# Kernel optimization log

Measured on AMD Instinct MI355X. Metric: run time of the kernel, lower is better.

## Reference

```python
import jax, jax.numpy as jnp
import numpy as np

EPS = 1e-10
TAU = 1.0


def setup_inputs() -> dict:
    key = jax.random.key(0)
    ks = jax.random.split(key, 5)
    n, d = 1024, 64
    h1, h2, out = 128, 64, 2
    X = jax.random.normal(ks[0], (n, d), dtype=jnp.float32)
    W1 = jax.random.normal(ks[1], (2 * d, h1), dtype=jnp.float32) * (1.0 / np.sqrt(2 * d))
    b1 = jnp.zeros((h1,), dtype=jnp.float32)
    W2 = jax.random.normal(ks[2], (h1, h2), dtype=jnp.float32) * (1.0 / np.sqrt(h1))
    b2 = jnp.zeros((h2,), dtype=jnp.float32)
    W3 = jax.random.normal(ks[3], (h2, out), dtype=jnp.float32) * (1.0 / np.sqrt(h2))
    b3 = jnp.zeros((out,), dtype=jnp.float32)
    u = jax.random.uniform(ks[4], (n, n, out), dtype=jnp.float32)
    return {"X": X, "W1": W1, "b1": b1, "W2": W2, "b2": b2, "W3": W3, "b3": b3, "u": u}


def _mlp(h, W1, b1, W2, b2, W3, b3):
    h = jax.nn.relu(h @ W1 + b1)
    h = jax.nn.relu(h @ W2 + b2)
    return h @ W3 + b3


def reference(X, W1, b1, W2, b2, W3, b3, u):
    n, d = X.shape
    # pairwise features: pair[i, j] = concat(x_i, x_j)  -> (n, n, 2d)
    pair = jnp.concatenate(
        [jnp.broadcast_to(X[:, None, :], (n, n, d)),
         jnp.broadcast_to(X[None, :, :], (n, n, d))], axis=-1)
    logits = _mlp(pair, W1, b1, W2, b2, W3, b3)  # (n, n, 2)
    # undirected: mlp(pair.permute(1,0,2))[i,j] == mlp(pair)[j,i] (row-wise MLP)
    logits = 0.5 * (logits + jnp.swapaxes(logits, 0, 1))
    # gumbel-softmax, hard=True (straight-through)
    g = -jnp.log(-jnp.log(u + EPS) + EPS)
    y_soft = jax.nn.softmax((logits + g) / TAU, axis=-1)
    y_hard = jax.nn.one_hot(jnp.argmax(y_soft, axis=-1), y_soft.shape[-1], dtype=y_soft.dtype)
    y = jax.lax.stop_gradient(y_hard - y_soft) + y_soft
    # narrow(dim=2, start=1, size=1).squeeze() -> adjacency (n, n)
    return y[..., 1]
```

## Files before the change

kernel.cpp:

```cpp
#include <hip/hip_runtime.h>
#include <hip/hip_bf16.h>

#define N 1024
#define D 64
#define H1 128
#define H2 64
#define FLAG_CAP 65536
#define FLAG_THRESH 0.015f
#define H1PAD 136

typedef _Float16 half8 __attribute__((ext_vector_type(8)));
typedef float float4v __attribute__((ext_vector_type(4)));

__global__ __launch_bounds__(128) void precompute_kernel(
    const float* __restrict__ X, const float* __restrict__ W1,
    const float* __restrict__ b1,
    double* __restrict__ A64, double* __restrict__ B64,
    _Float16* __restrict__ A16, _Float16* __restrict__ B16,
    unsigned int* __restrict__ cnt)
{
    if (blockIdx.x == 0 && threadIdx.x == 0) *cnt = 0;
    int i = blockIdx.x;
    int k = threadIdx.x;
    double a = (double)b1[k];
    double b = 0.0;
    for (int c = 0; c < D; ++c) {
        double x = (double)X[i * D + c];
        a += x * (double)W1[c * H1 + k];
        b += x * (double)W1[(D + c) * H1 + k];
    }
    A64[i * H1 + k] = a;
    B64[i * H1 + k] = b;
    A16[i * H1 + k] = (_Float16)(float)a;
    B16[i * H1 + k] = (_Float16)(float)b;
}

__global__ __launch_bounds__(256, 3) void pair_mlp_kernel(
    const _Float16* __restrict__ A16, const _Float16* __restrict__ B16,
    const float* __restrict__ W2, const float* __restrict__ b2,
    const float* __restrict__ W3, float* __restrict__ dmat)
{
    __shared__ _Float16 As16[16 * H1PAD];
    __shared__ _Float16 Bs16[64 * H1PAD];
    __shared__ _Float16 W2t[64 * H1PAD];

    int tid = threadIdx.x;
    int it = blockIdx.x >> 4;
    int jt = blockIdx.x & 15;
    int ti = it << 4;
    int tj = jt << 6;

    {
        int row = tid >> 4;
        int col = (tid & 15) << 3;
        *(half8*)&As16[row * H1PAD + col] =
            *(const half8*)&A16[(size_t)(ti + row) * H1 + col];
    }
    #pragma unroll
    for (int r = 0; r < 4; ++r) {
        int v = tid + r * 256;
        int row = v >> 4;
        int col = (v & 15) << 3;
        *(half8*)&Bs16[row * H1PAD + col] =
            *(const half8*)&B16[(size_t)(tj + row) * H1 + col];
    }
    #pragma unroll
    for (int r = 0; r < 32; ++r) {
        int idx = tid + r * 256;
        int k = idx >> 6;
        int n = idx & 63;
        W2t[n * H1PAD + k] = (_Float16)W2[idx];
    }
    __syncthreads();

    int lane = tid & 63;
    int wave = tid >> 6;
    int quad = lane >> 4;
    int m = lane & 15;

    half8 afrag[4][4];
    #pragma unroll
    for (int ks = 0; ks < 4; ++ks)
        #pragma unroll
        for (int nt = 0; nt < 4; ++nt)
            afrag[ks][nt] = *(const half8*)&W2t[(m + 16 * nt) * H1PAD + quad * 8 + 32 * ks];

    float b2x[4][4], w3x[4][4];
    #pragma unroll
    for (int nt = 0; nt < 4; ++nt)
        #pragma unroll
        for (int reg = 0; reg < 4; ++reg) {
            int o = (quad << 2) + reg + (nt << 4);
            b2x[nt][reg] = b2[o];
            w3x[nt][reg] = W3[o * 2 + 1] - W3[o * 2 + 0];
        }

    const half8 zero8 = {0, 0, 0, 0, 0, 0, 0, 0};

    #pragma unroll 1
    for (int jq = 0; jq < 4; ++jq) {
        int jj0 = jq << 4;
        half8 hb[4];
        #pragma unroll
        for (int ks = 0; ks < 4; ++ks)
            hb[ks] = *(const half8*)&Bs16[(jj0 + m) * H1PAD + quad * 8 + 32 * ks];

        #pragma unroll 1
        for (int i4 = 0; i4 < 4; ++i4) {
            int ii = (wave << 2) + i4;

            float4v acc[4];
            #pragma unroll
            for (int nt = 0; nt < 4; ++nt)
                acc[nt] = (float4v){b2x[nt][0], b2x[nt][1], b2x[nt][2], b2x[nt][3]};

            #pragma unroll
            for (int ks = 0; ks < 4; ++ks) {
                half8 ha = *(const half8*)&As16[ii * H1PAD + quad * 8 + 32 * ks];
                half8 h = __builtin_elementwise_max(ha + hb[ks], zero8);
                #pragma unroll
                for (int nt = 0; nt < 4; ++nt)
                    acc[nt] = __builtin_amdgcn_mfma_f32_16x16x32_f16(afrag[ks][nt], h, acc[nt], 0, 0, 0);
            }

            float s = 0.f;
            #pragma unroll
            for (int nt = 0; nt < 4; ++nt)
                #pragma unroll
                for (int reg = 0; reg < 4; ++reg)
                    s = fmaf(fmaxf(acc[nt][reg], 0.f), w3x[nt][reg], s);
            s += __shfl_xor(s, 16, 64);
            s += __shfl_xor(s, 32, 64);
            if (quad == 0) {
                dmat[(size_t)(ti + ii) * N + (tj + jj0 + m)] = s;
            }
        }
    }
}

__global__ __launch_bounds__(256) void epilogue_kernel(
    const float* __restrict__ dmat, const float* __restrict__ b3,
    const float* __restrict__ u,
    float* __restrict__ out, unsigned int* __restrict__ cnt,
    unsigned int* __restrict__ list)
{
    __shared__ float T1[32][33];
    __shared__ float T2[32][33];
    __shared__ unsigned int lflags[1024];
    __shared__ unsigned int lcnt, lbase;

    int bi = blockIdx.x >> 5;
    int bj = blockIdx.x & 31;
    int i0 = bi * 32, j0 = bj * 32;
    int tid = threadIdx.x;
    int r = tid >> 3;
    int c4 = (tid & 7) << 2;
    if (tid == 0) lcnt = 0;
    *(float4*)&T1[r][c4] = *(const float4*)&dmat[(size_t)(i0 + r) * N + j0 + c4];
    *(float4*)&T2[r][c4] = *(const float4*)&dmat[(size_t)(j0 + r) * N + i0 + c4];
    __syncthreads();

    float b3d = b3[1] - b3[0];
    int a = tid >> 3;
    int b0 = (tid & 7) << 2;
    int ij0 = (i0 + a) * N + (j0 + b0);

    float4 u01 = *(const float4*)&u[((size_t)ij0) * 2];
    float4 u23 = *(const float4*)&u[((size_t)ij0) * 2 + 4];
    float uu[8] = {u01.x, u01.y, u01.z, u01.w, u23.x, u23.y, u23.z, u23.w};

    float4 res;
    float* resp = &res.x;
    #pragma unroll
    for (int q = 0; q < 4; ++q) {
        int b = b0 + q;
        float g0 = -logf(-logf(uu[2 * q] + 1e-10f) + 1e-10f);
        float g1 = -logf(-logf(uu[2 * q + 1] + 1e-10f) + 1e-10f);
        float Dv = 0.5f * (T1[a][b] + T2[b][a]) + b3d + (g1 - g0);
        resp[q] = Dv > 0.f ? 1.f : 0.f;
        if (fabsf(Dv) < FLAG_THRESH) {
            unsigned int idx = atomicAdd(&lcnt, 1u);
            lflags[idx] = (unsigned int)(ij0 + q);
        }
    }
    *(float4*)&out[ij0] = res;

    __syncthreads();
    if (tid == 0) lbase = atomicAdd(cnt, lcnt);
    __syncthreads();
    unsigned int nl = lcnt, base = lbase;
    for (unsigned int k = tid; k < nl; k += 256) {
        unsigned int g = base + k;
        if (g < FLAG_CAP) list[g] = lflags[k];
    }
}

__global__ __launch_bounds__(64) void repair_kernel(
    const double* __restrict__ A64, const double* __restrict__ B64,
    const float* __restrict__ W2, const float* __restrict__ b2,
    const float* __restrict__ W3, const float* __restrict__ b3,
    const float* __restrict__ u,
    float* __restrict__ out, const unsigned int* __restrict__ cnt,
    const unsigned int* __restrict__ list)
{
    __shared__ double h1s[2][H1];
    int lane = threadIdx.x;

    unsigned int n = *cnt;
    if (n > FLAG_CAP) n = FLAG_CAP;
    double w3dd = (double)W3[lane * 2 + 1] - (double)W3[lane * 2 + 0];
    double b2d = (double)b2[lane];

    for (unsigned int f = blockIdx.x; f < n; f += gridDim.x) {
        int ij = (int)list[f];
        int i = ij >> 10, j = ij & (N - 1);
        {
            int k0 = lane, k1 = lane + 64;
            double ai0 = A64[(size_t)i * H1 + k0], ai1 = A64[(size_t)i * H1 + k1];
            double aj0 = A64[(size_t)j * H1 + k0], aj1 = A64[(size_t)j * H1 + k1];
            double bi0 = B64[(size_t)i * H1 + k0], bi1 = B64[(size_t)i * H1 + k1];
            double bj0 = B64[(size_t)j * H1 + k0], bj1 = B64[(size_t)j * H1 + k1];
            double v;
            v = ai0 + bj0; h1s[0][k0] = v > 0.0 ? v : 0.0;
            v = ai1 + bj1; h1s[0][k1] = v > 0.0 ? v : 0.0;
            v = aj0 + bi0; h1s[1][k0] = v > 0.0 ? v : 0.0;
            v = aj1 + bi1; h1s[1][k1] = v > 0.0 ? v : 0.0;
        }
        __syncthreads();
        double sa = b2d, sb = b2d;
        #pragma unroll 4
        for (int k = 0; k < H1; ++k) {
            double w = (double)W2[k * H2 + lane];
            sa += h1s[0][k] * w;
            sb += h1s[1][k] * w;
        }
        if (sa < 0.0) sa = 0.0;
        if (sb < 0.0) sb = 0.0;
        double da = sa * w3dd;
        double db = sb * w3dd;
        #pragma unroll
        for (int off = 32; off > 0; off >>= 1) {
            da += __shfl_down(da, off, 64);
            db += __shfl_down(db, off, 64);
        }
        if (lane == 0) {
            double b3dd = (double)b3[1] - (double)b3[0];
            double u0 = (double)u[(((size_t)ij) << 1) + 0];
            double u1 = (double)u[(((size_t)ij) << 1) + 1];
            double g0 = -log(-log(u0 + 1e-10) + 1e-10);
            double g1 = -log(-log(u1 + 1e-10) + 1e-10);
            double Dv = 0.5 * (da + db) + b3dd + (g1 - g0);
            out[ij] = Dv > 0.0 ? 1.f : 0.f;
        }
        __syncthreads();
    }
}

extern "C" void kernel_launch(void* const* d_in, const int* in_sizes, int n_in,
                              void* d_out, int out_size, void* d_ws, size_t ws_size,
                              hipStream_t stream) {
    const float* X  = (const float*)d_in[0];
    const float* W1 = (const float*)d_in[1];
    const float* b1 = (const float*)d_in[2];
    const float* W2 = (const float*)d_in[3];
    const float* b2 = (const float*)d_in[4];
    const float* W3 = (const float*)d_in[5];
    const float* b3 = (const float*)d_in[6];
    const float* u  = (const float*)d_in[7];
    float* out = (float*)d_out;

    double* A64 = (double*)d_ws;
    double* B64 = A64 + (size_t)N * H1;
    float* dmat = (float*)(B64 + (size_t)N * H1);
    _Float16* A16 = (_Float16*)(dmat + (size_t)N * N);
    _Float16* B16 = A16 + (size_t)N * H1;
    unsigned int* list = (unsigned int*)(B16 + (size_t)N * H1);
    unsigned int* cnt = list + FLAG_CAP;

    precompute_kernel<<<N, 128, 0, stream>>>(X, W1, b1, A64, B64, A16, B16, cnt);
    pair_mlp_kernel<<<(N / 16) * (N / 64), 256, 0, stream>>>(A16, B16, W2, b2, W3, dmat);
    epilogue_kernel<<<(N / 32) * (N / 32), 256, 0, stream>>>(dmat, b3, u, out, cnt, list);
    repair_kernel<<<2048, 64, 0, stream>>>(A64, B64, W2, b2, W3, b3, u, out, cnt, list);
}
```

Measured before the change: 147.1 us.

## Fuse flagged-pair double-precision repair into epilogue kernel, drop global list

Merges the repair pass into the epilogue: each block re-evaluates its own near-threshold pairs in double precision using four waves over its shared-memory flag list. This removes the global atomic counter, the flag list buffer and a separate kernel launch. The Gumbel log calls also switch to fast __logf intrinsics. The cost is more shared memory per epilogue block, and blocks with many flags now serialize repair work inside the block.

```diff
diff --git a/kernel.cpp b/kernel.cpp
--- a/kernel.cpp
+++ b/kernel.cpp
@@ -5,7 +5,6 @@
 #define D 64
 #define H1 128
 #define H2 64
-#define FLAG_CAP 65536
 #define FLAG_THRESH 0.015f
 #define H1PAD 136
 
@@ -16,10 +15,8 @@
     const float* __restrict__ X, const float* __restrict__ W1,
     const float* __restrict__ b1,
     double* __restrict__ A64, double* __restrict__ B64,
-    _Float16* __restrict__ A16, _Float16* __restrict__ B16,
-    unsigned int* __restrict__ cnt)
+    _Float16* __restrict__ A16, _Float16* __restrict__ B16)
 {
-    if (blockIdx.x == 0 && threadIdx.x == 0) *cnt = 0;
     int i = blockIdx.x;
     int k = threadIdx.x;
     double a = (double)b1[k];
@@ -138,16 +135,18 @@
     }
 }
 
-__global__ __launch_bounds__(256) void epilogue_kernel(
-    const float* __restrict__ dmat, const float* __restrict__ b3,
-    const float* __restrict__ u,
-    float* __restrict__ out, unsigned int* __restrict__ cnt,
-    unsigned int* __restrict__ list)
+__global__ __launch_bounds__(256) void epilogue_repair_kernel(
+    const float* __restrict__ dmat, const double* __restrict__ A64,
+    const double* __restrict__ B64, const float* __restrict__ W2,
+    const float* __restrict__ b2, const float* __restrict__ W3,
+    const float* __restrict__ b3, const float* __restrict__ u,
+    float* __restrict__ out)
 {
     __shared__ float T1[32][33];
     __shared__ float T2[32][33];
     __shared__ unsigned int lflags[1024];
-    __shared__ unsigned int lcnt, lbase;
+    __shared__ unsigned int lcnt;
+    __shared__ double h1s[4][2][H1];
 
     int bi = blockIdx.x >> 5;
     int bj = blockIdx.x & 31;
@@ -174,8 +173,8 @@
     #pragma unroll
     for (int q = 0; q < 4; ++q) {
         int b = b0 + q;
-        float g0 = -logf(-logf(uu[2 * q] + 1e-10f) + 1e-10f);
-        float g1 = -logf(-logf(uu[2 * q + 1] + 1e-10f) + 1e-10f);
+        float g0 = -__logf(-__logf(uu[2 * q] + 1e-10f) + 1e-10f);
+        float g1 = -__logf(-__logf(uu[2 * q + 1] + 1e-10f) + 1e-10f);
         float Dv = 0.5f * (T1[a][b] + T2[b][a]) + b3d + (g1 - g0);
         resp[q] = Dv > 0.f ? 1.f : 0.f;
         if (fabsf(Dv) < FLAG_THRESH) {
@@ -186,53 +185,39 @@
     *(float4*)&out[ij0] = res;
 
     __syncthreads();
-    if (tid == 0) lbase = atomicAdd(cnt, lcnt);
-    __syncthreads();
-    unsigned int nl = lcnt, base = lbase;
-    for (unsigned int k = tid; k < nl; k += 256) {
-        unsigned int g = base + k;
-        if (g < FLAG_CAP) list[g] = lflags[k];
-    }
-}
-
-__global__ __launch_bounds__(64) void repair_kernel(
-    const double* __restrict__ A64, const double* __restrict__ B64,
-    const float* __restrict__ W2, const float* __restrict__ b2,
-    const float* __restrict__ W3, const float* __restrict__ b3,
-    const float* __restrict__ u,
-    float* __restrict__ out, const unsigned int* __restrict__ cnt,
-    const unsigned int* __restrict__ list)
-{
-    __shared__ double h1s[2][H1];
-    int lane = threadIdx.x;
-
-    unsigned int n = *cnt;
-    if (n > FLAG_CAP) n = FLAG_CAP;
+    unsigned int nl = lcnt;
+    if (nl == 0) return;
+
+    int lane = tid & 63;
+    int wave = tid >> 6;
     double w3dd = (double)W3[lane * 2 + 1] - (double)W3[lane * 2 + 0];
     double b2d = (double)b2[lane];
-
-    for (unsigned int f = blockIdx.x; f < n; f += gridDim.x) {
-        int ij = (int)list[f];
+    int rounds = (int)((nl + 3) >> 2);
+
+    for (int t = 0; t < rounds; ++t) {
+        unsigned int f = ((unsigned)t << 2) + wave;
+        bool active = f < nl;
+        int ij = active ? (int)lflags[f] : 0;
         int i = ij >> 10, j = ij & (N - 1);
-        {
+        if (active) {
             int k0 = lane, k1 = lane + 64;
             double ai0 = A64[(size_t)i * H1 + k0], ai1 = A64[(size_t)i * H1 + k1];
             double aj0 = A64[(size_t)j * H1 + k0], aj1 = A64[(size_t)j * H1 + k1];
             double bi0 = B64[(size_t)i * H1 + k0], bi1 = B64[(size_t)i * H1 + k1];
             double bj0 = B64[(size_t)j * H1 + k0], bj1 = B64[(size_t)j * H1 + k1];
             double v;
-            v = ai0 + bj0; h1s[0][k0] = v > 0.0 ? v : 0.0;
-            v = ai1 + bj1; h1s[0][k1] = v > 0.0 ? v : 0.0;
-            v = aj0 + bi0; h1s[1][k0] = v > 0.0 ? v : 0.0;
-            v = aj1 + bi1; h1s[1][k1] = v > 0.0 ? v : 0.0;
+            v = ai0 + bj0; h1s[wave][0][k0] = v > 0.0 ? v : 0.0;
+            v = ai1 + bj1; h1s[wave][0][k1] = v > 0.0 ? v : 0.0;
+            v = aj0 + bi0; h1s[wave][1][k0] = v > 0.0 ? v : 0.0;
+            v = aj1 + bi1; h1s[wave][1][k1] = v > 0.0 ? v : 0.0;
         }
         __syncthreads();
         double sa = b2d, sb = b2d;
         #pragma unroll 4
         for (int k = 0; k < H1; ++k) {
             double w = (double)W2[k * H2 + lane];
-            sa += h1s[0][k] * w;
-            sb += h1s[1][k] * w;
+            sa += h1s[wave][0][k] * w;
+            sb += h1s[wave][1][k] * w;
         }
         if (sa < 0.0) sa = 0.0;
         if (sb < 0.0) sb = 0.0;
@@ -243,7 +228,7 @@
             da += __shfl_down(da, off, 64);
             db += __shfl_down(db, off, 64);
         }
-        if (lane == 0) {
+        if (active && lane == 0) {
             double b3dd = (double)b3[1] - (double)b3[0];
             double u0 = (double)u[(((size_t)ij) << 1) + 0];
             double u1 = (double)u[(((size_t)ij) << 1) + 1];
@@ -274,11 +259,9 @@
     float* dmat = (float*)(B64 + (size_t)N * H1);
     _Float16* A16 = (_Float16*)(dmat + (size_t)N * N);
     _Float16* B16 = A16 + (size_t)N * H1;
-    unsigned int* list = (unsigned int*)(B16 + (size_t)N * H1);
-    unsigned int* cnt = list + FLAG_CAP;
-
-    precompute_kernel<<<N, 128, 0, stream>>>(X, W1, b1, A64, B64, A16, B16, cnt);
+
+    precompute_kernel<<<N, 128, 0, stream>>>(X, W1, b1, A64, B64, A16, B16);
     pair_mlp_kernel<<<(N / 16) * (N / 64), 256, 0, stream>>>(A16, B16, W2, b2, W3, dmat);
-    epilogue_kernel<<<(N / 32) * (N / 32), 256, 0, stream>>>(dmat, b3, u, out, cnt, list);
-    repair_kernel<<<2048, 64, 0, stream>>>(A64, B64, W2, b2, W3, b3, u, out, cnt, list);
-}
+    epilogue_repair_kernel<<<(N / 32) * (N / 32), 256, 0, stream>>>(
+        dmat, A64, B64, W2, b2, W3, b3, u, out);
+}
```

After: 142.5 us. 1.03x faster.
